# Performance work log

Measured on AMD Instinct MI355X. Metric: run time of the kernel, lower is better.

Reference implementation:

```python
import jax, jax.numpy as jnp
import numpy as np

T, C, H = 2048, 1024, 16
D = C // H  # head dim = 64


def setup_inputs() -> dict:
    key = jax.random.key(0)
    k1, k2, k3 = jax.random.split(key, 3)
    x = jax.random.normal(k1, (T, C), dtype=jnp.float32)
    W_qkv = jax.random.normal(k2, (C, 3 * C), dtype=jnp.float32) * (1.0 / np.sqrt(C))
    b_qkv = jnp.zeros((3 * C,), dtype=jnp.float32)
    W_proj = jax.random.normal(k3, (C, C), dtype=jnp.float32) * (1.0 / np.sqrt(C))
    b_proj = jnp.zeros((C,), dtype=jnp.float32)
    return {"x": x, "W_qkv": W_qkv, "b_qkv": b_qkv, "W_proj": W_proj, "b_proj": b_proj}


def reference(x, W_qkv, b_qkv, W_proj, b_proj):
    t, c = x.shape
    qkv = x @ W_qkv + b_qkv                      # [T, 3C] fused QKV projection
    q, k, v = jnp.split(qkv, 3, axis=-1)         # each [T, C]
    # split heads: [T, C] -> [H, T, D]
    q = q.reshape(t, H, D).transpose(1, 0, 2)
    k = k.reshape(t, H, D).transpose(1, 0, 2)
    v = v.reshape(t, H, D).transpose(1, 0, 2)
    # naive O(T^2) attention, full score matrix [H, T, T]
    att = jnp.einsum('htd,hsd->hts', q, k) / jnp.sqrt(jnp.float32(D))
    att = jax.nn.softmax(att, axis=-1)
    y = jnp.einsum('hts,hsd->htd', att, v)       # [H, T, D]
    y = y.transpose(1, 0, 2).reshape(t, c)       # merge heads -> [T, C]
    return y @ W_proj + b_proj
```

## Files before the change

### kernel.cpp

```cpp
#include <hip/hip_runtime.h>
#include <hip/hip_bf16.h>
#include <stdint.h>

#define T_DIM 2048
#define C_DIM 1024
#define H_DIM 16
#define D_HEAD 64
#define N_QKV 3072
#define CQ 0.18033688011112042f

typedef __bf16 bf16;
typedef __bf16 bf16x8 __attribute__((ext_vector_type(8)));
typedef __bf16 bf16x4 __attribute__((ext_vector_type(4)));
typedef float f32x4 __attribute__((ext_vector_type(4)));
typedef short s16x4 __attribute__((ext_vector_type(4)));

__device__ __forceinline__ void lds_load16(const void* g, void* l) {
    __builtin_amdgcn_global_load_lds(
        (const __attribute__((address_space(1))) void*)g,
        (__attribute__((address_space(3))) void*)l, 16, 0, 0);
}

__device__ __forceinline__ f32x4 mfma16(bf16x4 a, bf16x4 b, f32x4 c) {
#if __has_builtin(__builtin_amdgcn_mfma_f32_16x16x16_bf16)
    return __builtin_amdgcn_mfma_f32_16x16x16_bf16(a, b, c, 0, 0, 0);
#elif __has_builtin(__builtin_amdgcn_mfma_f32_16x16x16bf16_1k)
    union { bf16x4 v; s16x4 s; } ua, ub;
    ua.v = a; ub.v = b;
    return __builtin_amdgcn_mfma_f32_16x16x16bf16_1k(ua.s, ub.s, c, 0, 0, 0);
#else
    asm volatile("v_mfma_f32_16x16x16_bf16 %0, %1, %2, %0"
                 : "+v"(c) : "v"(a), "v"(b));
    return c;
#endif
}

__global__ void cast_bf16_kernel(const float* __restrict__ in, bf16* __restrict__ out, int n) {
    int i = (blockIdx.x * 256 + threadIdx.x) * 8;
    if (i >= n) return;
    float4 a = *(const float4*)(in + i);
    float4 b = *(const float4*)(in + i + 4);
    bf16x8 o;
    o[0] = (bf16)a.x; o[1] = (bf16)a.y; o[2] = (bf16)a.z; o[3] = (bf16)a.w;
    o[4] = (bf16)b.x; o[5] = (bf16)b.y; o[6] = (bf16)b.z; o[7] = (bf16)b.w;
    *(bf16x8*)(out + i) = o;
}

__global__ void cast_transpose2_kernel(const float* __restrict__ Wq, bf16* __restrict__ WqT,
                                       const float* __restrict__ Wp, bf16* __restrict__ WpT) {
    __shared__ float tile[32][33];
    int bid = blockIdx.x;
    const float* in; bf16* out; int N, nb, kb;
    if (bid < 3072) { in = Wq; out = WqT; N = N_QKV; nb = (bid % 96) * 32; kb = (bid / 96) * 32; }
    else { bid -= 3072; in = Wp; out = WpT; N = C_DIM; nb = (bid % 32) * 32; kb = (bid / 32) * 32; }
    int t = threadIdx.x;
    int r = t >> 3, c4 = (t & 7) * 4;
    float4 v = *(const float4*)(in + (size_t)(kb + r) * N + nb + c4);
    tile[r][c4 + 0] = v.x; tile[r][c4 + 1] = v.y;
    tile[r][c4 + 2] = v.z; tile[r][c4 + 3] = v.w;
    __syncthreads();
    bf16x4 ov;
    ov[0] = (bf16)tile[c4 + 0][r]; ov[1] = (bf16)tile[c4 + 1][r];
    ov[2] = (bf16)tile[c4 + 2][r]; ov[3] = (bf16)tile[c4 + 3][r];
    *(bf16x4*)(out + (size_t)(nb + r) * C_DIM + kb + c4) = ov;
}

__global__ __launch_bounds__(256) void qkv_gemm_kernel(
    const bf16* __restrict__ A, const bf16* __restrict__ Bt,
    const float* __restrict__ bias, bf16* __restrict__ qkv)
{
    __shared__ __align__(16) bf16 As[128 * 32];
    __shared__ __align__(16) bf16 Bs[128 * 32];
    const int tid = threadIdx.x, lane = tid & 63, w = tid >> 6;
    const int lo16 = lane & 15, quad = lane >> 4;
    const int wm = (w & 1) * 64, wn = (w >> 1) * 64;
    const int rowBase = blockIdx.y * 128, colBase = blockIdx.x * 128;

    const bf16* ga = A  + (size_t)(rowBase + w * 16 + (lane >> 2)) * C_DIM + (lane & 3) * 8;
    const bf16* gb = Bt + (size_t)(colBase + w * 16 + (lane >> 2)) * C_DIM + (lane & 3) * 8;
    bf16* laA0 = &As[(w * 16) * 32];
    bf16* laA1 = &As[(64 + w * 16) * 32];
    bf16* lbB0 = &Bs[(w * 16) * 32];
    bf16* lbB1 = &Bs[(64 + w * 16) * 32];

    f32x4 acc[4][4] = {};

    for (int k0 = 0; k0 < C_DIM; k0 += 32) {
        __syncthreads();
        lds_load16(ga + k0, laA0);
        lds_load16(ga + (size_t)64 * C_DIM + k0, laA1);
        lds_load16(gb + k0, lbB0);
        lds_load16(gb + (size_t)64 * C_DIM + k0, lbB1);
        __syncthreads();
        bf16x8 af[4], bfr[4];
        #pragma unroll
        for (int mi = 0; mi < 4; ++mi) af[mi]  = *(const bf16x8*)&As[(wm + mi * 16 + lo16) * 32 + quad * 8];
        #pragma unroll
        for (int ni = 0; ni < 4; ++ni) bfr[ni] = *(const bf16x8*)&Bs[(wn + ni * 16 + lo16) * 32 + quad * 8];
        #pragma unroll
        for (int mi = 0; mi < 4; ++mi)
            #pragma unroll
            for (int ni = 0; ni < 4; ++ni)
                acc[mi][ni] = __builtin_amdgcn_mfma_f32_16x16x32_bf16(af[mi], bfr[ni], acc[mi][ni], 0, 0, 0);
    }

    const float scale = (colBase < C_DIM) ? CQ : 1.0f;
    #pragma unroll
    for (int ni = 0; ni < 4; ++ni) {
        int col = colBase + wn + ni * 16 + lo16;
        float bv = bias[col];
        #pragma unroll
        for (int mi = 0; mi < 4; ++mi) {
            int row0 = rowBase + wm + mi * 16 + quad * 4;
            #pragma unroll
            for (int r = 0; r < 4; ++r)
                qkv[(size_t)(row0 + r) * N_QKV + col] = (bf16)((acc[mi][ni][r] + bv) * scale);
        }
    }
}

__global__ __launch_bounds__(256, 3) void flash_kernel(
    const bf16* __restrict__ qkv,
    bf16* __restrict__ y)
{
    __shared__ union {
        __align__(16) bf16 Vt[2][64][40];
        float Ored[4][16][66];
    } u;
    __shared__ float lred[4][64];

    const int h = blockIdx.x, qb = blockIdx.y;
    const int tid  = threadIdx.x;
    const int lane = tid & 63, w = tid >> 6;
    const int lo16 = lane & 15, quad = lane >> 4;

    bf16x8 qf[4][2];
    #pragma unroll
    for (int nq = 0; nq < 4; ++nq)
        #pragma unroll
        for (int dk = 0; dk < 2; ++dk)
            qf[nq][dk] = *(const bf16x8*)(qkv + (size_t)(qb * 64 + nq * 16 + lo16) * N_QKV
                                          + h * D_HEAD + dk * 32 + quad * 8);

    f32x4 o_t[4][4] = {};
    float l_acc[4] = {};

    const bf16* kfb = qkv + (size_t)(w * 16 + lo16) * N_QKV + C_DIM + h * D_HEAD + quad * 8;
    const unsigned short* vb16 = (const unsigned short*)(qkv + 2 * C_DIM + h * D_HEAD);

    bf16x8 kf0 = *(const bf16x8*)(kfb);
    bf16x8 kf1 = *(const bf16x8*)(kfb + 32);
    unsigned short vreg[16];
    #pragma unroll
    for (int i = 0; i < 16; ++i)
        vreg[i] = vb16[(size_t)(w * 16 + i) * N_QKV + lane];

    bf16* vdst = &u.Vt[w >> 1][lane][(w & 1) * 16];

    for (int kt = 0; kt < T_DIM / 64; ++kt) {
        union { bf16x8 v; unsigned short us[8]; } p0, p1;
        #pragma unroll
        for (int i = 0; i < 8; ++i) { p0.us[i] = vreg[i]; p1.us[i] = vreg[8 + i]; }
        *(bf16x8*)vdst       = p0.v;
        *(bf16x8*)(vdst + 8) = p1.v;

        bf16x8 nkf0 = kf0, nkf1 = kf1;
        if (kt + 1 < T_DIM / 64) {
            const bf16* kp = kfb + (size_t)(kt + 1) * 64 * N_QKV;
            nkf0 = *(const bf16x8*)(kp);
            nkf1 = *(const bf16x8*)(kp + 32);
            #pragma unroll
            for (int i = 0; i < 16; ++i)
                vreg[i] = vb16[(size_t)((kt + 1) * 64 + w * 16 + i) * N_QKV + lane];
        }

        f32x4 st[4];
        #pragma unroll
        for (int nq = 0; nq < 4; ++nq) {
            f32x4 z = {};
            z = __builtin_amdgcn_mfma_f32_16x16x32_bf16(kf0, qf[nq][0], z, 0, 0, 0);
            st[nq] = __builtin_amdgcn_mfma_f32_16x16x32_bf16(kf1, qf[nq][1], z, 0, 0, 0);
        }

        bf16x4 pb[4];
        #pragma unroll
        for (int nq = 0; nq < 4; ++nq)
            #pragma unroll
            for (int r = 0; r < 4; ++r) {
                float p = __builtin_amdgcn_exp2f(st[nq][r]);
                l_acc[nq] += p;
                pb[nq][r] = (bf16)p;
            }

        bf16x4 vf[4];
        #pragma unroll
        for (int mi = 0; mi < 4; ++mi)
            vf[mi] = *(const bf16x4*)&u.Vt[w >> 1][mi * 16 + lo16][(w & 1) * 16 + quad * 4];

        #pragma unroll
        for (int mi = 0; mi < 4; ++mi)
            #pragma unroll
            for (int nq = 0; nq < 4; ++nq)
                o_t[mi][nq] = mfma16(vf[mi], pb[nq], o_t[mi][nq]);

        kf0 = nkf0; kf1 = nkf1;
    }

    #pragma unroll
    for (int nq = 0; nq < 4; ++nq) {
        l_acc[nq] += __shfl_xor(l_acc[nq], 16);
        l_acc[nq] += __shfl_xor(l_acc[nq], 32);
        if (quad == 0) lred[w][nq * 16 + lo16] = l_acc[nq];
    }

    const int q = tid & 63, dg = tid >> 6;
    float linv = 0.f;
    #pragma unroll
    for (int mi = 0; mi < 4; ++mi) {
        __syncthreads();
        #pragma unroll
        for (int nq = 0; nq < 4; ++nq)
            #pragma unroll
            for (int r = 0; r < 4; ++r)
                u.Ored[w][quad * 4 + r][nq * 16 + lo16] = o_t[mi][nq][r];
        __syncthreads();
        if (mi == 0)
            linv = 1.0f / (lred[0][q] + lred[1][q] + lred[2][q] + lred[3][q]);
        bf16x4 ov;
        #pragma unroll
        for (int dj = 0; dj < 4; ++dj) {
            int d = dg * 4 + dj;
            ov[dj] = (bf16)((u.Ored[0][d][q] + u.Ored[1][d][q] + u.Ored[2][d][q] + u.Ored[3][d][q]) * linv);
        }
        *(bf16x4*)&y[(size_t)(qb * 64 + q) * C_DIM + h * D_HEAD + mi * 16 + dg * 4] = ov;
    }
}

__global__ __launch_bounds__(256) void proj_gemm_kernel(
    const bf16* __restrict__ A, const bf16* __restrict__ Bt,
    const float* __restrict__ bias, float* __restrict__ out)
{
    __shared__ __align__(16) bf16 As[128 * 32];
    __shared__ __align__(16) bf16 Bs[64 * 32];
    const int tid = threadIdx.x, lane = tid & 63, w = tid >> 6;
    const int lo16 = lane & 15, quad = lane >> 4;
    const int wm = (w & 1) * 64, wn = (w >> 1) * 32;
    const int rowBase = blockIdx.y * 128, colBase = blockIdx.x * 64;

    const bf16* ga = A  + (size_t)(rowBase + w * 16 + (lane >> 2)) * C_DIM + (lane & 3) * 8;
    const bf16* gb = Bt + (size_t)(colBase + w * 16 + (lane >> 2)) * C_DIM + (lane & 3) * 8;
    bf16* laA0 = &As[(w * 16) * 32];
    bf16* laA1 = &As[(64 + w * 16) * 32];
    bf16* lbB  = &Bs[(w * 16) * 32];

    f32x4 acc[4][2] = {};

    for (int k0 = 0; k0 < C_DIM; k0 += 32) {
        __syncthreads();
        lds_load16(ga + k0, laA0);
        lds_load16(ga + (size_t)64 * C_DIM + k0, laA1);
        lds_load16(gb + k0, lbB);
        __syncthreads();
        bf16x8 af[4], bfr[2];
        #pragma unroll
        for (int mi = 0; mi < 4; ++mi) af[mi]  = *(const bf16x8*)&As[(wm + mi * 16 + lo16) * 32 + quad * 8];
        #pragma unroll
        for (int ni = 0; ni < 2; ++ni) bfr[ni] = *(const bf16x8*)&Bs[(wn + ni * 16 + lo16) * 32 + quad * 8];
        #pragma unroll
        for (int mi = 0; mi < 4; ++mi)
            #pragma unroll
            for (int ni = 0; ni < 2; ++ni)
                acc[mi][ni] = __builtin_amdgcn_mfma_f32_16x16x32_bf16(af[mi], bfr[ni], acc[mi][ni], 0, 0, 0);
    }

    #pragma unroll
    for (int ni = 0; ni < 2; ++ni) {
        int col = colBase + wn + ni * 16 + lo16;
        float bv = bias[col];
        #pragma unroll
        for (int mi = 0; mi < 4; ++mi) {
            int row0 = rowBase + wm + mi * 16 + quad * 4;
            #pragma unroll
            for (int r = 0; r < 4; ++r)
                out[(size_t)(row0 + r) * C_DIM + col] = acc[mi][ni][r] + bv;
        }
    }
}

extern "C" void kernel_launch(void* const* d_in, const int* in_sizes, int n_in,
                              void* d_out, int out_size, void* d_ws, size_t ws_size,
                              hipStream_t stream) {
    const float* x      = (const float*)d_in[0];
    const float* W_qkv  = (const float*)d_in[1];
    const float* b_qkv  = (const float*)d_in[2];
    const float* W_proj = (const float*)d_in[3];
    const float* b_proj = (const float*)d_in[4];
    float* out = (float*)d_out;

    char* ws = (char*)d_ws;
    bf16* xb      = (bf16*)(ws);
    bf16* Wqkv_t  = (bf16*)(ws + (4  << 20));
    bf16* Wproj_t = (bf16*)(ws + (10 << 20));
    bf16* qkv_bf  = (bf16*)(ws + (12 << 20));
    bf16* yb      = (bf16*)(ws + (24 << 20));

    cast_bf16_kernel<<<(T_DIM * C_DIM) / (256 * 8), 256, 0, stream>>>(x, xb, T_DIM * C_DIM);
    cast_transpose2_kernel<<<4096, 256, 0, stream>>>(W_qkv, Wqkv_t, W_proj, Wproj_t);

    qkv_gemm_kernel<<<dim3(N_QKV / 128, T_DIM / 128), 256, 0, stream>>>(
        xb, Wqkv_t, b_qkv, qkv_bf);

    flash_kernel<<<dim3(H_DIM, T_DIM / 64), 256, 0, stream>>>(qkv_bf, yb);

    proj_gemm_kernel<<<dim3(C_DIM / 64, T_DIM / 128), 256, 0, stream>>>(
        yb, Wproj_t, b_proj, out);
}
```

Baseline: 155.5 us.

## Retile QKV and proj GEMMs with K=64 stages and use 8-wave flash blocks

The QKV GEMM moves to 128x64 tiles and the projection GEMM to 64x64 tiles. Both now stage 64 K-elements per barrier pair, which halves the number of syncs and launches more blocks for better CU fill. The flash kernel goes to 512 threads (8 waves), so each block covers 128 keys per iteration, and the final reduction now sums 8 partial outputs. Smaller GEMM tiles lower data reuse per block, and the wider flash block raises LDS use and reduction cost.

```diff
diff --git a/kernel.cpp b/kernel.cpp
--- a/kernel.cpp
+++ b/kernel.cpp
@@ -12,6 +12,7 @@
 typedef __bf16 bf16;
 typedef __bf16 bf16x8 __attribute__((ext_vector_type(8)));
 typedef __bf16 bf16x4 __attribute__((ext_vector_type(4)));
+typedef __bf16 bf16x2 __attribute__((ext_vector_type(2)));
 typedef float f32x4 __attribute__((ext_vector_type(4)));
 typedef short s16x4 __attribute__((ext_vector_type(4)));
 
@@ -65,48 +66,49 @@
     *(bf16x4*)(out + (size_t)(nb + r) * C_DIM + kb + c4) = ov;
 }
 
-__global__ __launch_bounds__(256) void qkv_gemm_kernel(
+__global__ __launch_bounds__(256, 3) void qkv_gemm_kernel(
     const bf16* __restrict__ A, const bf16* __restrict__ Bt,
     const float* __restrict__ bias, bf16* __restrict__ qkv)
 {
-    __shared__ __align__(16) bf16 As[128 * 32];
-    __shared__ __align__(16) bf16 Bs[128 * 32];
+    __shared__ __align__(16) bf16 As[2][128 * 32];
+    __shared__ __align__(16) bf16 Bs[2][64 * 32];
     const int tid = threadIdx.x, lane = tid & 63, w = tid >> 6;
     const int lo16 = lane & 15, quad = lane >> 4;
-    const int wm = (w & 1) * 64, wn = (w >> 1) * 64;
-    const int rowBase = blockIdx.y * 128, colBase = blockIdx.x * 128;
+    const int wm = (w & 1) * 64, wn = (w >> 1) * 32;
+    const int rowBase = blockIdx.y * 128, colBase = blockIdx.x * 64;
 
     const bf16* ga = A  + (size_t)(rowBase + w * 16 + (lane >> 2)) * C_DIM + (lane & 3) * 8;
     const bf16* gb = Bt + (size_t)(colBase + w * 16 + (lane >> 2)) * C_DIM + (lane & 3) * 8;
-    bf16* laA0 = &As[(w * 16) * 32];
-    bf16* laA1 = &As[(64 + w * 16) * 32];
-    bf16* lbB0 = &Bs[(w * 16) * 32];
-    bf16* lbB1 = &Bs[(64 + w * 16) * 32];
-
-    f32x4 acc[4][4] = {};
-
-    for (int k0 = 0; k0 < C_DIM; k0 += 32) {
-        __syncthreads();
-        lds_load16(ga + k0, laA0);
-        lds_load16(ga + (size_t)64 * C_DIM + k0, laA1);
-        lds_load16(gb + k0, lbB0);
-        lds_load16(gb + (size_t)64 * C_DIM + k0, lbB1);
-        __syncthreads();
-        bf16x8 af[4], bfr[4];
-        #pragma unroll
-        for (int mi = 0; mi < 4; ++mi) af[mi]  = *(const bf16x8*)&As[(wm + mi * 16 + lo16) * 32 + quad * 8];
-        #pragma unroll
-        for (int ni = 0; ni < 4; ++ni) bfr[ni] = *(const bf16x8*)&Bs[(wn + ni * 16 + lo16) * 32 + quad * 8];
-        #pragma unroll
-        for (int mi = 0; mi < 4; ++mi)
-            #pragma unroll
-            for (int ni = 0; ni < 4; ++ni)
-                acc[mi][ni] = __builtin_amdgcn_mfma_f32_16x16x32_bf16(af[mi], bfr[ni], acc[mi][ni], 0, 0, 0);
+
+    f32x4 acc[4][2] = {};
+
+    for (int k0 = 0; k0 < C_DIM; k0 += 64) {
+        __syncthreads();
+        #pragma unroll
+        for (int p = 0; p < 2; ++p) {
+            lds_load16(ga + k0 + p * 32, &As[p][(w * 16) * 32]);
+            lds_load16(ga + (size_t)64 * C_DIM + k0 + p * 32, &As[p][(64 + w * 16) * 32]);
+            lds_load16(gb + k0 + p * 32, &Bs[p][(w * 16) * 32]);
+        }
+        __syncthreads();
+        #pragma unroll
+        for (int p = 0; p < 2; ++p) {
+            bf16x8 af[4], bfr[2];
+            #pragma unroll
+            for (int mi = 0; mi < 4; ++mi) af[mi]  = *(const bf16x8*)&As[p][(wm + mi * 16 + lo16) * 32 + quad * 8];
+            #pragma unroll
+            for (int ni = 0; ni < 2; ++ni) bfr[ni] = *(const bf16x8*)&Bs[p][(wn + ni * 16 + lo16) * 32 + quad * 8];
+            #pragma unroll
+            for (int mi = 0; mi < 4; ++mi)
+                #pragma unroll
+                for (int ni = 0; ni < 2; ++ni)
+                    acc[mi][ni] = __builtin_amdgcn_mfma_f32_16x16x32_bf16(af[mi], bfr[ni], acc[mi][ni], 0, 0, 0);
+        }
     }
 
     const float scale = (colBase < C_DIM) ? CQ : 1.0f;
     #pragma unroll
-    for (int ni = 0; ni < 4; ++ni) {
+    for (int ni = 0; ni < 2; ++ni) {
         int col = colBase + wn + ni * 16 + lo16;
         float bv = bias[col];
         #pragma unroll
@@ -119,15 +121,15 @@
     }
 }
 
-__global__ __launch_bounds__(256, 3) void flash_kernel(
+__global__ __launch_bounds__(512, 2) void flash_kernel(
     const bf16* __restrict__ qkv,
     bf16* __restrict__ y)
 {
     __shared__ union {
-        __align__(16) bf16 Vt[2][64][40];
-        float Ored[4][16][66];
+        __align__(16) bf16 Vt[4][64][38];
+        float Ored[8][16][66];
     } u;
-    __shared__ float lred[4][64];
+    __shared__ float lred[8][64];
 
     const int h = blockIdx.x, qb = blockIdx.y;
     const int tid  = threadIdx.x;
@@ -157,7 +159,7 @@
 
     bf16* vdst = &u.Vt[w >> 1][lane][(w & 1) * 16];
 
-    for (int kt = 0; kt < T_DIM / 64; ++kt) {
+    for (int kt = 0; kt < T_DIM / 128; ++kt) {
         union { bf16x8 v; unsigned short us[8]; } p0, p1;
         #pragma unroll
         for (int i = 0; i < 8; ++i) { p0.us[i] = vreg[i]; p1.us[i] = vreg[8 + i]; }
@@ -165,13 +167,13 @@
         *(bf16x8*)(vdst + 8) = p1.v;
 
         bf16x8 nkf0 = kf0, nkf1 = kf1;
-        if (kt + 1 < T_DIM / 64) {
-            const bf16* kp = kfb + (size_t)(kt + 1) * 64 * N_QKV;
+        if (kt + 1 < T_DIM / 128) {
+            const bf16* kp = kfb + (size_t)(kt + 1) * 128 * N_QKV;
             nkf0 = *(const bf16x8*)(kp);
             nkf1 = *(const bf16x8*)(kp + 32);
             #pragma unroll
             for (int i = 0; i < 16; ++i)
-                vreg[i] = vb16[(size_t)((kt + 1) * 64 + w * 16 + i) * N_QKV + lane];
+                vreg[i] = vb16[(size_t)((kt + 1) * 128 + w * 16 + i) * N_QKV + lane];
         }
 
         f32x4 st[4];
@@ -213,7 +215,7 @@
         if (quad == 0) lred[w][nq * 16 + lo16] = l_acc[nq];
     }
 
-    const int q = tid & 63, dg = tid >> 6;
+    const int q8 = tid >> 3, dh = tid & 7;
     float linv = 0.f;
     #pragma unroll
     for (int mi = 0; mi < 4; ++mi) {
@@ -224,53 +226,62 @@
             for (int r = 0; r < 4; ++r)
                 u.Ored[w][quad * 4 + r][nq * 16 + lo16] = o_t[mi][nq][r];
         __syncthreads();
-        if (mi == 0)
-            linv = 1.0f / (lred[0][q] + lred[1][q] + lred[2][q] + lred[3][q]);
-        bf16x4 ov;
-        #pragma unroll
-        for (int dj = 0; dj < 4; ++dj) {
-            int d = dg * 4 + dj;
-            ov[dj] = (bf16)((u.Ored[0][d][q] + u.Ored[1][d][q] + u.Ored[2][d][q] + u.Ored[3][d][q]) * linv);
-        }
-        *(bf16x4*)&y[(size_t)(qb * 64 + q) * C_DIM + h * D_HEAD + mi * 16 + dg * 4] = ov;
-    }
-}
-
-__global__ __launch_bounds__(256) void proj_gemm_kernel(
+        if (mi == 0) {
+            float ls = 0.f;
+            #pragma unroll
+            for (int j = 0; j < 8; ++j) ls += lred[j][q8];
+            linv = 1.0f / ls;
+        }
+        bf16x2 ov;
+        #pragma unroll
+        for (int dj = 0; dj < 2; ++dj) {
+            int d = dh * 2 + dj;
+            float s = 0.f;
+            #pragma unroll
+            for (int j = 0; j < 8; ++j) s += u.Ored[j][d][q8];
+            ov[dj] = (bf16)(s * linv);
+        }
+        *(bf16x2*)&y[(size_t)(qb * 64 + q8) * C_DIM + h * D_HEAD + mi * 16 + dh * 2] = ov;
+    }
+}
+
+__global__ __launch_bounds__(256, 4) void proj_gemm_kernel(
     const bf16* __restrict__ A, const bf16* __restrict__ Bt,
     const float* __restrict__ bias, float* __restrict__ out)
 {
-    __shared__ __align__(16) bf16 As[128 * 32];
-    __shared__ __align__(16) bf16 Bs[64 * 32];
+    __shared__ __align__(16) bf16 As[2][64 * 32];
+    __shared__ __align__(16) bf16 Bs[2][64 * 32];
     const int tid = threadIdx.x, lane = tid & 63, w = tid >> 6;
     const int lo16 = lane & 15, quad = lane >> 4;
-    const int wm = (w & 1) * 64, wn = (w >> 1) * 32;
-    const int rowBase = blockIdx.y * 128, colBase = blockIdx.x * 64;
+    const int wm = (w & 1) * 32, wn = (w >> 1) * 32;
+    const int rowBase = blockIdx.y * 64, colBase = blockIdx.x * 64;
 
     const bf16* ga = A  + (size_t)(rowBase + w * 16 + (lane >> 2)) * C_DIM + (lane & 3) * 8;
     const bf16* gb = Bt + (size_t)(colBase + w * 16 + (lane >> 2)) * C_DIM + (lane & 3) * 8;
-    bf16* laA0 = &As[(w * 16) * 32];
-    bf16* laA1 = &As[(64 + w * 16) * 32];
-    bf16* lbB  = &Bs[(w * 16) * 32];
-
-    f32x4 acc[4][2] = {};
-
-    for (int k0 = 0; k0 < C_DIM; k0 += 32) {
-        __syncthreads();
-        lds_load16(ga + k0, laA0);
-        lds_load16(ga + (size_t)64 * C_DIM + k0, laA1);
-        lds_load16(gb + k0, lbB);
-        __syncthreads();
-        bf16x8 af[4], bfr[2];
-        #pragma unroll
-        for (int mi = 0; mi < 4; ++mi) af[mi]  = *(const bf16x8*)&As[(wm + mi * 16 + lo16) * 32 + quad * 8];
-        #pragma unroll
-        for (int ni = 0; ni < 2; ++ni) bfr[ni] = *(const bf16x8*)&Bs[(wn + ni * 16 + lo16) * 32 + quad * 8];
-        #pragma unroll
-        for (int mi = 0; mi < 4; ++mi)
-            #pragma unroll
-            for (int ni = 0; ni < 2; ++ni)
-                acc[mi][ni] = __builtin_amdgcn_mfma_f32_16x16x32_bf16(af[mi], bfr[ni], acc[mi][ni], 0, 0, 0);
+
+    f32x4 acc[2][2] = {};
+
+    for (int k0 = 0; k0 < C_DIM; k0 += 64) {
+        __syncthreads();
+        #pragma unroll
+        for (int p = 0; p < 2; ++p) {
+            lds_load16(ga + k0 + p * 32, &As[p][(w * 16) * 32]);
+            lds_load16(gb + k0 + p * 32, &Bs[p][(w * 16) * 32]);
+        }
+        __syncthreads();
+        #pragma unroll
+        for (int p = 0; p < 2; ++p) {
+            bf16x8 af[2], bfr[2];
+            #pragma unroll
+            for (int mi = 0; mi < 2; ++mi) af[mi]  = *(const bf16x8*)&As[p][(wm + mi * 16 + lo16) * 32 + quad * 8];
+            #pragma unroll
+            for (int ni = 0; ni < 2; ++ni) bfr[ni] = *(const bf16x8*)&Bs[p][(wn + ni * 16 + lo16) * 32 + quad * 8];
+            #pragma unroll
+            for (int mi = 0; mi < 2; ++mi)
+                #pragma unroll
+                for (int ni = 0; ni < 2; ++ni)
+                    acc[mi][ni] = __builtin_amdgcn_mfma_f32_16x16x32_bf16(af[mi], bfr[ni], acc[mi][ni], 0, 0, 0);
+        }
     }
 
     #pragma unroll
@@ -278,7 +289,7 @@
         int col = colBase + wn + ni * 16 + lo16;
         float bv = bias[col];
         #pragma unroll
-        for (int mi = 0; mi < 4; ++mi) {
+        for (int mi = 0; mi < 2; ++mi) {
             int row0 = rowBase + wm + mi * 16 + quad * 4;
             #pragma unroll
             for (int r = 0; r < 4; ++r)
@@ -307,11 +318,11 @@
     cast_bf16_kernel<<<(T_DIM * C_DIM) / (256 * 8), 256, 0, stream>>>(x, xb, T_DIM * C_DIM);
     cast_transpose2_kernel<<<4096, 256, 0, stream>>>(W_qkv, Wqkv_t, W_proj, Wproj_t);
 
-    qkv_gemm_kernel<<<dim3(N_QKV / 128, T_DIM / 128), 256, 0, stream>>>(
+    qkv_gemm_kernel<<<dim3(N_QKV / 64, T_DIM / 128), 256, 0, stream>>>(
         xb, Wqkv_t, b_qkv, qkv_bf);
 
-    flash_kernel<<<dim3(H_DIM, T_DIM / 64), 256, 0, stream>>>(qkv_bf, yb);
-
-    proj_gemm_kernel<<<dim3(C_DIM / 64, T_DIM / 128), 256, 0, stream>>>(
+    flash_kernel<<<dim3(H_DIM, T_DIM / 64), 512, 0, stream>>>(qkv_bf, yb);
+
+    proj_gemm_kernel<<<dim3(C_DIM / 64, T_DIM / 64), 256, 0, stream>>>(
         yb, Wproj_t, b_proj, out);
 }
```

Result: faster. 148.8 us (-4.3%).
